# Kernel tuning notes

Hardware: AMD Instinct MI355X
Metric: run time of the kernel (lower is better)

## Reference

```python
import jax, jax.numpy as jnp
import numpy as np

WIN = 8      # window size
HEADS = 8    # num attention heads
LN_EPS = 1e-5


def setup_inputs() -> dict:
    key = jax.random.key(0)
    ks = jax.random.split(key, 4)
    B, C, H, W = 4, 256, 224, 224
    x = jax.random.normal(ks[0], (B, C, H, W), jnp.float32)
    # LayerNorm params (torch default init: weight=1, bias=0)
    ln_gamma = jnp.ones((C,), jnp.float32)
    ln_beta = jnp.zeros((C,), jnp.float32)
    # nn.MultiheadAttention: in_proj_weight xavier_uniform, biases zero
    s_in = float(np.sqrt(6.0 / (C + 3 * C)))
    w_qkv = jax.random.uniform(ks[1], (3 * C, C), jnp.float32, -s_in, s_in)
    b_qkv = jnp.zeros((3 * C,), jnp.float32)
    s_out = float(np.sqrt(6.0 / (C + C)))
    w_out = jax.random.uniform(ks[2], (C, C), jnp.float32, -s_out, s_out)
    b_out = jnp.zeros((C,), jnp.float32)
    return {"x": x, "ln_gamma": ln_gamma, "ln_beta": ln_beta,
            "w_qkv": w_qkv, "b_qkv": b_qkv, "w_out": w_out, "b_out": b_out}


def reference(x, ln_gamma, ln_beta, w_qkv, b_qkv, w_out, b_out):
    B, C, H, W = x.shape
    w = WIN
    h = HEADS
    d = C // h
    T = w * w  # tokens per window (64)
    # (B,C,H,W) -> (B,H,W,C); H,W divisible by win_size so F.pad is a no-op
    xb = jnp.transpose(x, (0, 2, 3, 1))
    # window_partition: (B*nW, T, C)
    win = xb.reshape(B, H // w, w, W // w, w, C)
    win = win.transpose(0, 1, 3, 2, 4, 5).reshape(-1, T, C)
    # LayerNorm over channel dim (same norm for q, k, v as in the source)
    mu = jnp.mean(win, axis=-1, keepdims=True)
    var = jnp.var(win, axis=-1, keepdims=True)  # biased, matches torch LN
    xn = (win - mu) * jax.lax.rsqrt(var + LN_EPS) * ln_gamma + ln_beta
    # fused QKV projection (torch MHA self-attn fast path)
    qkv = xn @ w_qkv.T + b_qkv          # (N, T, 3C)
    q, k, v = jnp.split(qkv, 3, axis=-1)

    def to_heads(t):  # (N, T, C) -> (N, h, T, d)
        return t.reshape(t.shape[0], T, h, d).transpose(0, 2, 1, 3)

    q, k, v = to_heads(q), to_heads(k), to_heads(v)
    scale = 1.0 / np.sqrt(d)
    scores = jnp.einsum('nhqd,nhkd->nhqk', q * scale, k)
    attn = jax.nn.softmax(scores, axis=-1)
    o = jnp.einsum('nhqk,nhkd->nhqd', attn, v)          # (N, h, T, d)
    o = o.transpose(0, 2, 1, 3).reshape(-1, T, C)       # merge heads
    o = o @ w_out.T + b_out
    # window_reverse: (B*nW, T, C) -> (B, H, W, C)
    out = o.reshape(B, H // w, W // w, w, w, C)
    out = out.transpose(0, 1, 3, 2, 4, 5).reshape(B, H, W, C)
    return jnp.transpose(out, (0, 3, 1, 2))  # (B, C, H, W)
```

## Files before the change

kernel.cpp:

```cpp
#include <hip/hip_runtime.h>
#include <hip/hip_fp16.h>

#define C_   256
#define H_   224
#define W_   224
#define HW_  (224 * 224)
#define NWH  28
#define NWW  28
#define NWIN 3136
#define NQUAD 784
#define NTILE 64
#define NFRAG (NTILE * 8 * 64)

#define XN_OFF (1ULL << 20)
#define O_OFF  (XN_OFF + (unsigned long long)NWIN * 32768ULL)
#define WS_NEED (O_OFF + (unsigned long long)NWIN * 32768ULL)

typedef _Float16 f16x8 __attribute__((ext_vector_type(8)));
typedef float    f32x4 __attribute__((ext_vector_type(4)));

__device__ __forceinline__ int xn_off(int row, int col) {
  return (row * 512 + col * 2) ^ ((((row & 7) ^ ((row >> 3) & 7))) << 4);
}
__device__ __forceinline__ int qk_off(int row, int col) {
  return (row * 64 + col * 2) ^ (((row >> 1) & 3) << 4);
}
__device__ __forceinline__ int vt_off(int d, int k) {
  return (d * 128 + k * 2) ^ ((d & 7) << 4);
}
__device__ __forceinline__ int p_off(int row, int col) {
  return (row * 128 + col * 2) ^ ((row & 7) << 4);
}
__device__ __forceinline__ _Float16* xn_at(char* s, int r, int c) { return (_Float16*)(s + xn_off(r, c)); }

__global__ void wcvt_kernel(const float* __restrict__ wqkv,
                            const float* __restrict__ wout,
                            _Float16* __restrict__ dst) {
  int f = blockIdx.x * blockDim.x + threadIdx.x;
  if (f >= NFRAG) return;
  int lane = f & 63, kk = (f >> 6) & 7, tile = f >> 9;
  int row = tile * 16 + (lane & 15);
  int col = kk * 32 + (lane >> 4) * 8;
  const float* src = (tile < 48) ? (wqkv + row * 256 + col)
                                 : (wout + (row - 768) * 256 + col);
  f32x4 a = *(const f32x4*)src;
  f32x4 b2 = *(const f32x4*)(src + 4);
  f16x8 r;
#pragma unroll
  for (int q = 0; q < 4; ++q) { r[q] = (_Float16)a[q]; r[q + 4] = (_Float16)b2[q]; }
  *(f16x8*)(dst + (size_t)f * 8) = r;
}

__global__ __launch_bounds__(512, 1) void prep_kernel(
    const float* __restrict__ x, const float* __restrict__ gamma,
    const float* __restrict__ beta, _Float16* __restrict__ xn_ws) {
  extern __shared__ char smem[];
  float* red = (float*)(smem + 131072);
  float* mrs = (float*)(smem + 147456);
  const int n0 = blockIdx.x;
  const int b  = n0 / 196;
  const int rem = n0 % 196;
  const int wh = rem / 7;
  const int wq = rem % 7;
  const int tid = threadIdx.x;
  const int px4 = (tid & 7) * 4;
  const int row = (tid >> 3) & 7;
  const int chg = tid >> 6;
  const int win = px4 >> 3;
  const int pc  = px4 & 7;
  char* xw = smem + win * 32768;

  {
    const size_t xoff = (size_t)b * C_ * HW_ + (size_t)(wh * 8 + row) * W_ + wq * 32 + px4;
    float s[4] = {0.f, 0.f, 0.f, 0.f}, q[4] = {0.f, 0.f, 0.f, 0.f};
#pragma unroll
    for (int cc = 0; cc < 32; ++cc) {
      const int ch = cc * 8 + chg;
      f32x4 v = *(const f32x4*)(x + xoff + (size_t)ch * HW_);
#pragma unroll
      for (int i = 0; i < 4; ++i) {
        *xn_at(xw, row * 8 + pc + i, ch) = (_Float16)v[i];
        s[i] += v[i]; q[i] += v[i] * v[i];
      }
    }
    const int tq = win * 64 + row * 8 + pc;
#pragma unroll
    for (int i = 0; i < 4; ++i) {
      red[(tq + i) * 8 + chg] = s[i];
      red[2048 + (tq + i) * 8 + chg] = q[i];
    }
  }
  __syncthreads();
  if (tid < 256) {
    float ss = 0.f, s2 = 0.f;
#pragma unroll
    for (int g = 0; g < 8; ++g) { ss += red[tid * 8 + g]; s2 += red[2048 + tid * 8 + g]; }
    float mu  = ss * (1.f / 256.f);
    float var = s2 * (1.f / 256.f) - mu * mu;
    mrs[tid]       = mu;
    mrs[256 + tid] = rsqrtf(var + 1e-5f);
  }
  __syncthreads();
  {
    char* dst = (char*)xn_ws + (size_t)((b * NWH + wh) * NWW + wq * 4) * 32768;
#pragma unroll
    for (int it = 0; it < 16; ++it) {
      const int a   = (it * 512 + tid) * 16;
      const int w2  = a >> 15;
      const int ab  = a & 32767;
      const int tok = ab >> 9;
      const int chb = ((ab & 511) ^ ((((tok & 7) ^ ((tok >> 3) & 7))) << 4)) >> 1;
      f16x8 hv = *(const f16x8*)(smem + a);
      const float mu = mrs[w2 * 64 + tok], rs = mrs[256 + w2 * 64 + tok];
      f32x4 g0 = *(const f32x4*)(gamma + chb), g1 = *(const f32x4*)(gamma + chb + 4);
      f32x4 b0 = *(const f32x4*)(beta + chb),  b1 = *(const f32x4*)(beta + chb + 4);
#pragma unroll
      for (int j = 0; j < 4; ++j) {
        hv[j]     = (_Float16)(((float)hv[j] - mu) * rs * g0[j] + b0[j]);
        hv[j + 4] = (_Float16)(((float)hv[j + 4] - mu) * rs * g1[j] + b1[j]);
      }
      *(f16x8*)(dst + a) = hv;
    }
  }
}

__global__ __launch_bounds__(512, 1) void megattn_kernel(
    const float* __restrict__ bqkv, const _Float16* __restrict__ w16,
    const _Float16* __restrict__ xn_ws, _Float16* __restrict__ o_ws) {
  extern __shared__ char smem[];
  const int tid = threadIdx.x;
  const int w = tid >> 6, lane = tid & 63, lr = lane & 15, lg = lane >> 4;
  const int winl = w >> 1;
  const int half = w & 1;
  const int r0   = half * 32;
  const int win  = blockIdx.x * 4 + winl;

  f16x8 af[2][8];
  {
    const char* xb = (const char*)xn_ws + (size_t)win * 32768;
#pragma unroll
    for (int mi = 0; mi < 2; ++mi)
#pragma unroll
      for (int kk = 0; kk < 8; ++kk)
        af[mi][kk] = *(const f16x8*)(xb + xn_off(r0 + mi * 16 + lr, kk * 32 + lg * 8));
  }

  char* scr   = smem + 49152 + winl * 12288;
  char* kbase = scr + 4096;
  char* vbase = scr + 8192;
  char* obuf  = smem + 98304 + winl * 4096;
  char* oblob = (char*)o_ws + (size_t)win * 32768;
  const float sc_q = 0.17677669529663687f;

#pragma unroll 1
  for (int h = 0; h < 8; ++h) {
    __syncthreads();
    {
      const char* s0 = (const char*)w16 + (size_t)(2 * h) * 8192;
      const char* s1 = (const char*)w16 + (size_t)(16 + 2 * h) * 8192;
      const char* s2 = (const char*)w16 + (size_t)(32 + 2 * h) * 8192;
#pragma unroll
      for (int it = 0; it < 2; ++it) {
        const int o = (it * 512 + tid) * 16;
        *(f32x4*)(smem + o)         = *(const f32x4*)(s0 + o);
        *(f32x4*)(smem + 16384 + o) = *(const f32x4*)(s1 + o);
        *(f32x4*)(smem + 32768 + o) = *(const f32x4*)(s2 + o);
      }
    }
    __syncthreads();

    f32x4 acc[6][2];
#pragma unroll
    for (int t = 0; t < 6; ++t)
#pragma unroll
      for (int mi = 0; mi < 2; ++mi) acc[t][mi] = (f32x4){0.f, 0.f, 0.f, 0.f};
#pragma unroll
    for (int kk = 0; kk < 8; ++kk) {
      const int fo = (kk * 64 + lane) * 16;
      f16x8 b0 = *(const f16x8*)(smem + fo);
      f16x8 b1 = *(const f16x8*)(smem + 8192 + fo);
      f16x8 b2 = *(const f16x8*)(smem + 16384 + fo);
      f16x8 b3 = *(const f16x8*)(smem + 24576 + fo);
      f16x8 b4 = *(const f16x8*)(smem + 32768 + fo);
      f16x8 b5 = *(const f16x8*)(smem + 40960 + fo);
#pragma unroll
      for (int mi = 0; mi < 2; ++mi) {
        acc[0][mi] = __builtin_amdgcn_mfma_f32_16x16x32_f16(af[mi][kk], b0, acc[0][mi], 0, 0, 0);
        acc[1][mi] = __builtin_amdgcn_mfma_f32_16x16x32_f16(af[mi][kk], b1, acc[1][mi], 0, 0, 0);
        acc[2][mi] = __builtin_amdgcn_mfma_f32_16x16x32_f16(af[mi][kk], b2, acc[2][mi], 0, 0, 0);
        acc[3][mi] = __builtin_amdgcn_mfma_f32_16x16x32_f16(af[mi][kk], b3, acc[3][mi], 0, 0, 0);
        acc[4][mi] = __builtin_amdgcn_mfma_f32_16x16x32_f16(af[mi][kk], b4, acc[4][mi], 0, 0, 0);
        acc[5][mi] = __builtin_amdgcn_mfma_f32_16x16x32_f16(af[mi][kk], b5, acc[5][mi], 0, 0, 0);
      }
    }
#pragma unroll
    for (int t2 = 0; t2 < 2; ++t2) {
      const float bq = bqkv[h * 32 + t2 * 16 + lr];
      const float bk = bqkv[256 + h * 32 + t2 * 16 + lr];
      const float bv = bqkv[512 + h * 32 + t2 * 16 + lr];
#pragma unroll
      for (int mi = 0; mi < 2; ++mi)
#pragma unroll
        for (int i = 0; i < 4; ++i) {
          const int trow = r0 + mi * 16 + lg * 4 + i;
          *(_Float16*)(scr + qk_off(trow, t2 * 16 + lr))   = (_Float16)((acc[t2][mi][i] + bq) * sc_q);
          *(_Float16*)(kbase + qk_off(trow, t2 * 16 + lr)) = (_Float16)(acc[2 + t2][mi][i] + bk);
          *(_Float16*)(vbase + vt_off(t2 * 16 + lr, trow)) = (_Float16)(acc[4 + t2][mi][i] + bv);
        }
    }
    __syncthreads();

    f16x8 qa[2], kb[4];
#pragma unroll
    for (int mi = 0; mi < 2; ++mi)
      qa[mi] = *(const f16x8*)(scr + qk_off(r0 + mi * 16 + lr, lg * 8));
#pragma unroll
    for (int ni = 0; ni < 4; ++ni)
      kb[ni] = *(const f16x8*)(kbase + qk_off(ni * 16 + lr, lg * 8));
    __syncthreads();

    float oinv[2][4];
#pragma unroll
    for (int mi = 0; mi < 2; ++mi) {
      f32x4 s4[4];
#pragma unroll
      for (int ni = 0; ni < 4; ++ni) {
        f32x4 z = {0.f, 0.f, 0.f, 0.f};
        s4[ni] = __builtin_amdgcn_mfma_f32_16x16x32_f16(qa[mi], kb[ni], z, 0, 0, 0);
      }
#pragma unroll
      for (int i = 0; i < 4; ++i) {
        float m = fmaxf(fmaxf(s4[0][i], s4[1][i]), fmaxf(s4[2][i], s4[3][i]));
        m = fmaxf(m, __shfl_xor(m, 1));
        m = fmaxf(m, __shfl_xor(m, 2));
        m = fmaxf(m, __shfl_xor(m, 4));
        m = fmaxf(m, __shfl_xor(m, 8));
        float s = 0.f;
#pragma unroll
        for (int ni = 0; ni < 4; ++ni) {
          float e = __expf(s4[ni][i] - m);
          s4[ni][i] = e;
          s += e;
        }
        s += __shfl_xor(s, 1);
        s += __shfl_xor(s, 2);
        s += __shfl_xor(s, 4);
        s += __shfl_xor(s, 8);
        oinv[mi][i] = 1.f / s;
      }
#pragma unroll
      for (int ni = 0; ni < 4; ++ni)
#pragma unroll
        for (int i = 0; i < 4; ++i)
          *(_Float16*)(scr + p_off(r0 + mi * 16 + lg * 4 + i, ni * 16 + lr)) = (_Float16)s4[ni][i];
    }
    f32x4 oacc[2][2];
#pragma unroll
    for (int mi = 0; mi < 2; ++mi)
#pragma unroll
      for (int nt2 = 0; nt2 < 2; ++nt2) oacc[mi][nt2] = (f32x4){0.f, 0.f, 0.f, 0.f};
#pragma unroll
    for (int ks2 = 0; ks2 < 2; ++ks2) {
      f16x8 pa[2];
#pragma unroll
      for (int mi = 0; mi < 2; ++mi)
        pa[mi] = *(const f16x8*)(scr + p_off(r0 + mi * 16 + lr, ks2 * 32 + lg * 8));
#pragma unroll
      for (int nt2 = 0; nt2 < 2; ++nt2) {
        f16x8 vb = *(const f16x8*)(vbase + vt_off(nt2 * 16 + lr, ks2 * 32 + lg * 8));
#pragma unroll
        for (int mi = 0; mi < 2; ++mi)
          oacc[mi][nt2] = __builtin_amdgcn_mfma_f32_16x16x32_f16(pa[mi], vb, oacc[mi][nt2], 0, 0, 0);
      }
    }
#pragma unroll
    for (int mi = 0; mi < 2; ++mi)
#pragma unroll
      for (int nt2 = 0; nt2 < 2; ++nt2)
#pragma unroll
        for (int i = 0; i < 4; ++i)
          *(_Float16*)(obuf + qk_off(r0 + mi * 16 + lg * 4 + i, nt2 * 16 + lr)) =
              (_Float16)(oacc[mi][nt2][i] * oinv[mi][i]);
#pragma unroll
    for (int j = 0; j < 2; ++j)
      *(f32x4*)(oblob + h * 4096 + half * 2048 + lane * 32 + j * 16) =
          *(const f32x4*)(obuf + half * 2048 + lane * 32 + j * 16);
  }
}

__device__ __forceinline__ f16x8 frag16(const _Float16* __restrict__ w16,
                                        int gt, int kk, int lane) {
  return *(const f16x8*)(w16 + ((size_t)((gt * 8 + kk) * 64 + lane)) * 8);
}
__global__ __launch_bounds__(512, 1) void outproj_kernel(
    const _Float16* __restrict__ o_ws, const _Float16* __restrict__ w16,
    const float* __restrict__ bout, float* __restrict__ out) {
  extern __shared__ char smem[];
  const int n0 = blockIdx.x;
  const int b  = n0 / 196;
  const int rem = n0 % 196;
  const int wh = rem / 7;
  const int wq = rem % 7;
  const int tid = threadIdx.x;
  const int w = tid >> 6, lane = tid & 63, lr = lane & 15, lg = lane >> 4;

  {
    const char* src = (const char*)o_ws + (size_t)((b * NWH + wh) * NWW + wq * 4) * 32768;
#pragma unroll
    for (int it = 0; it < 16; ++it) {
      const int off = (it * 512 + tid) * 16;
      *(f32x4*)(smem + off) = *(const f32x4*)(src + off);
    }
  }
  __syncthreads();

  f32x4 acc[4][2][4];
#pragma unroll
  for (int wi = 0; wi < 4; ++wi)
#pragma unroll
    for (int t = 0; t < 2; ++t)
#pragma unroll
      for (int mi = 0; mi < 4; ++mi) acc[wi][t][mi] = (f32x4){0.f, 0.f, 0.f, 0.f};

#pragma unroll
  for (int kk = 0; kk < 8; ++kk) {
    f16x8 bf0 = frag16(w16, 48 + w * 2 + 0, kk, lane);
    f16x8 bf1 = frag16(w16, 48 + w * 2 + 1, kk, lane);
#pragma unroll
    for (int wi = 0; wi < 4; ++wi) {
      f16x8 af[4];
#pragma unroll
      for (int mi = 0; mi < 4; ++mi)
        af[mi] = *(const f16x8*)(smem + wi * 32768 + kk * 4096 + qk_off(mi * 16 + lr, lg * 8));
#pragma unroll
      for (int mi = 0; mi < 4; ++mi) {
        acc[wi][0][mi] = __builtin_amdgcn_mfma_f32_16x16x32_f16(af[mi], bf0, acc[wi][0][mi], 0, 0, 0);
        acc[wi][1][mi] = __builtin_amdgcn_mfma_f32_16x16x32_f16(af[mi], bf1, acc[wi][1][mi], 0, 0, 0);
      }
    }
  }

#pragma unroll
  for (int ntl = 0; ntl < 2; ++ntl) {
    const int och = w * 32 + ntl * 16 + lr;
    const float bias = bout[och];
    float* ob = out + ((size_t)(b * C_ + och) * H_ + wh * 8) * W_ + wq * 32;
#pragma unroll
    for (int mi = 0; mi < 4; ++mi) {
      const int tb = mi * 16 + lg * 4;
      const int ro = (tb >> 3) * W_ + (tb & 7);
#pragma unroll
      for (int wi = 0; wi < 4; ++wi) {
        f32x4 ov;
#pragma unroll
        for (int i = 0; i < 4; ++i) ov[i] = acc[wi][ntl][mi][i] + bias;
        *(f32x4*)&ob[ro + wi * 8] = ov;
      }
    }
  }
}

extern "C" void kernel_launch(void* const* d_in, const int* in_sizes, int n_in,
                              void* d_out, int out_size, void* d_ws, size_t ws_size,
                              hipStream_t stream) {
  (void)in_sizes; (void)n_in; (void)out_size; (void)ws_size;
  const float* x     = (const float*)d_in[0];
  const float* gamma = (const float*)d_in[1];
  const float* beta  = (const float*)d_in[2];
  const float* wqkv  = (const float*)d_in[3];
  const float* bqkv  = (const float*)d_in[4];
  const float* wout  = (const float*)d_in[5];
  const float* bout  = (const float*)d_in[6];
  float* out = (float*)d_out;

  _Float16* w16   = (_Float16*)d_ws;
  _Float16* xn_ws = (_Float16*)((char*)d_ws + XN_OFF);
  _Float16* o_ws  = (_Float16*)((char*)d_ws + O_OFF);

  static int attr_set = 0;
  if (!attr_set) {
    (void)hipFuncSetAttribute((const void*)prep_kernel,
                              hipFuncAttributeMaxDynamicSharedMemorySize, 149504);
    (void)hipFuncSetAttribute((const void*)megattn_kernel,
                              hipFuncAttributeMaxDynamicSharedMemorySize, 114688);
    (void)hipFuncSetAttribute((const void*)outproj_kernel,
                              hipFuncAttributeMaxDynamicSharedMemorySize, 131072);
    attr_set = 1;
  }

  wcvt_kernel<<<NFRAG / 256, 256, 0, stream>>>(wqkv, wout, w16);
  prep_kernel<<<NQUAD, 512, 149504, stream>>>(x, gamma, beta, xn_ws);
  megattn_kernel<<<NQUAD, 512, 114688, stream>>>(bqkv, w16, xn_ws, o_ws);
  outproj_kernel<<<NQUAD, 512, 131072, stream>>>(o_ws, w16, bout, out);
}
```

Before: 411.8 us.

## Read QKV weight fragments from global memory and shrink attention blocks for occupancy

```diff
diff --git a/kernel.cpp b/kernel.cpp
--- a/kernel.cpp
+++ b/kernel.cpp
@@ -32,6 +32,11 @@
   return (row * 128 + col * 2) ^ ((row & 7) << 4);
 }
 __device__ __forceinline__ _Float16* xn_at(char* s, int r, int c) { return (_Float16*)(s + xn_off(r, c)); }
+
+__device__ __forceinline__ f16x8 frag16(const _Float16* __restrict__ w16,
+                                        int gt, int kk, int lane) {
+  return *(const f16x8*)(w16 + ((size_t)((gt * 8 + kk) * 64 + lane)) * 8);
+}
 
 __global__ void wcvt_kernel(const float* __restrict__ wqkv,
                             const float* __restrict__ wout,
@@ -124,7 +129,7 @@
   }
 }
 
-__global__ __launch_bounds__(512, 1) void megattn_kernel(
+__global__ __launch_bounds__(256, 4) void megattn_kernel(
     const float* __restrict__ bqkv, const _Float16* __restrict__ w16,
     const _Float16* __restrict__ xn_ws, _Float16* __restrict__ o_ws) {
   extern __shared__ char smem[];
@@ -133,7 +138,7 @@
   const int winl = w >> 1;
   const int half = w & 1;
   const int r0   = half * 32;
-  const int win  = blockIdx.x * 4 + winl;
+  const int win  = blockIdx.x * 2 + winl;
 
   f16x8 af[2][8];
   {
@@ -145,30 +150,15 @@
         af[mi][kk] = *(const f16x8*)(xb + xn_off(r0 + mi * 16 + lr, kk * 32 + lg * 8));
   }
 
-  char* scr   = smem + 49152 + winl * 12288;
+  char* scr   = smem + winl * 12288;
   char* kbase = scr + 4096;
   char* vbase = scr + 8192;
-  char* obuf  = smem + 98304 + winl * 4096;
+  char* obuf  = smem + 24576 + winl * 4096;
   char* oblob = (char*)o_ws + (size_t)win * 32768;
   const float sc_q = 0.17677669529663687f;
 
 #pragma unroll 1
   for (int h = 0; h < 8; ++h) {
-    __syncthreads();
-    {
-      const char* s0 = (const char*)w16 + (size_t)(2 * h) * 8192;
-      const char* s1 = (const char*)w16 + (size_t)(16 + 2 * h) * 8192;
-      const char* s2 = (const char*)w16 + (size_t)(32 + 2 * h) * 8192;
-#pragma unroll
-      for (int it = 0; it < 2; ++it) {
-        const int o = (it * 512 + tid) * 16;
-        *(f32x4*)(smem + o)         = *(const f32x4*)(s0 + o);
-        *(f32x4*)(smem + 16384 + o) = *(const f32x4*)(s1 + o);
-        *(f32x4*)(smem + 32768 + o) = *(const f32x4*)(s2 + o);
-      }
-    }
-    __syncthreads();
-
     f32x4 acc[6][2];
 #pragma unroll
     for (int t = 0; t < 6; ++t)
@@ -176,13 +166,12 @@
       for (int mi = 0; mi < 2; ++mi) acc[t][mi] = (f32x4){0.f, 0.f, 0.f, 0.f};
 #pragma unroll
     for (int kk = 0; kk < 8; ++kk) {
-      const int fo = (kk * 64 + lane) * 16;
-      f16x8 b0 = *(const f16x8*)(smem + fo);
-      f16x8 b1 = *(const f16x8*)(smem + 8192 + fo);
-      f16x8 b2 = *(const f16x8*)(smem + 16384 + fo);
-      f16x8 b3 = *(const f16x8*)(smem + 24576 + fo);
-      f16x8 b4 = *(const f16x8*)(smem + 32768 + fo);
-      f16x8 b5 = *(const f16x8*)(smem + 40960 + fo);
+      f16x8 b0 = frag16(w16, 2 * h,      kk, lane);
+      f16x8 b1 = frag16(w16, 2 * h + 1,  kk, lane);
+      f16x8 b2 = frag16(w16, 16 + 2 * h, kk, lane);
+      f16x8 b3 = frag16(w16, 17 + 2 * h, kk, lane);
+      f16x8 b4 = frag16(w16, 32 + 2 * h, kk, lane);
+      f16x8 b5 = frag16(w16, 33 + 2 * h, kk, lane);
 #pragma unroll
       for (int mi = 0; mi < 2; ++mi) {
         acc[0][mi] = __builtin_amdgcn_mfma_f32_16x16x32_f16(af[mi][kk], b0, acc[0][mi], 0, 0, 0);
@@ -193,6 +182,8 @@
         acc[5][mi] = __builtin_amdgcn_mfma_f32_16x16x32_f16(af[mi][kk], b5, acc[5][mi], 0, 0, 0);
       }
     }
+    __syncthreads();
+
 #pragma unroll
     for (int t2 = 0; t2 < 2; ++t2) {
       const float bq = bqkv[h * 32 + t2 * 16 + lr];
@@ -288,10 +279,6 @@
   }
 }
 
-__device__ __forceinline__ f16x8 frag16(const _Float16* __restrict__ w16,
-                                        int gt, int kk, int lane) {
-  return *(const f16x8*)(w16 + ((size_t)((gt * 8 + kk) * 64 + lane)) * 8);
-}
 __global__ __launch_bounds__(512, 1) void outproj_kernel(
     const _Float16* __restrict__ o_ws, const _Float16* __restrict__ w16,
     const float* __restrict__ bout, float* __restrict__ out) {
@@ -382,7 +369,7 @@
     (void)hipFuncSetAttribute((const void*)prep_kernel,
                               hipFuncAttributeMaxDynamicSharedMemorySize, 149504);
     (void)hipFuncSetAttribute((const void*)megattn_kernel,
-                              hipFuncAttributeMaxDynamicSharedMemorySize, 114688);
+                              hipFuncAttributeMaxDynamicSharedMemorySize, 32768);
     (void)hipFuncSetAttribute((const void*)outproj_kernel,
                               hipFuncAttributeMaxDynamicSharedMemorySize, 131072);
     attr_set = 1;
@@ -390,6 +377,6 @@
 
   wcvt_kernel<<<NFRAG / 256, 256, 0, stream>>>(wqkv, wout, w16);
   prep_kernel<<<NQUAD, 512, 149504, stream>>>(x, gamma, beta, xn_ws);
-  megattn_kernel<<<NQUAD, 512, 114688, stream>>>(bqkv, w16, xn_ws, o_ws);
+  megattn_kernel<<<NWIN / 2, 256, 32768, stream>>>(bqkv, w16, xn_ws, o_ws);
   outproj_kernel<<<NQUAD, 512, 131072, stream>>>(o_ws, w16, bout, out);
 }
```

After: 816.6 us. +98.3%, slower.

## Double-buffer per-head QKV weight tiles in LDS with register prefetch

Applied to the files above, without the earlier changes.

```diff
diff --git a/kernel.cpp b/kernel.cpp
--- a/kernel.cpp
+++ b/kernel.cpp
@@ -32,6 +32,17 @@
   return (row * 128 + col * 2) ^ ((row & 7) << 4);
 }
 __device__ __forceinline__ _Float16* xn_at(char* s, int r, int c) { return (_Float16*)(s + xn_off(r, c)); }
+
+__device__ __forceinline__ f16x8 frag16(const _Float16* __restrict__ w16,
+                                        int gt, int kk, int lane) {
+  return *(const f16x8*)(w16 + ((size_t)((gt * 8 + kk) * 64 + lane)) * 8);
+}
+
+__device__ __forceinline__ const char* wsrc(const char* w16b, int h, int c, int lane) {
+  const int reg = c >> 4;
+  const int off = (c & 15) << 10;
+  return w16b + (size_t)(reg * 16 + 2 * h) * 8192 + off + lane * 16;
+}
 
 __global__ void wcvt_kernel(const float* __restrict__ wqkv,
                             const float* __restrict__ wout,
@@ -134,6 +145,7 @@
   const int half = w & 1;
   const int r0   = half * 32;
   const int win  = blockIdx.x * 4 + winl;
+  const char* w16b = (const char*)w16;
 
   f16x8 af[2][8];
   {
@@ -145,30 +157,34 @@
         af[mi][kk] = *(const f16x8*)(xb + xn_off(r0 + mi * 16 + lr, kk * 32 + lg * 8));
   }
 
-  char* scr   = smem + 49152 + winl * 12288;
+  char* scr   = smem + 98304 + winl * 12288;
   char* kbase = scr + 4096;
   char* vbase = scr + 8192;
-  char* obuf  = smem + 98304 + winl * 4096;
+  char* obuf  = smem + 147456 + winl * 4096;
   char* oblob = (char*)o_ws + (size_t)win * 32768;
   const float sc_q = 0.17677669529663687f;
 
+  {
+    f32x4 r[6];
+#pragma unroll
+    for (int i = 0; i < 6; ++i)
+      r[i] = *(const f32x4*)wsrc(w16b, 0, w * 6 + i, lane);
+#pragma unroll
+    for (int i = 0; i < 6; ++i)
+      *(f32x4*)(smem + (w * 6 + i) * 1024 + lane * 16) = r[i];
+  }
+  __syncthreads();
+
 #pragma unroll 1
   for (int h = 0; h < 8; ++h) {
-    __syncthreads();
-    {
-      const char* s0 = (const char*)w16 + (size_t)(2 * h) * 8192;
-      const char* s1 = (const char*)w16 + (size_t)(16 + 2 * h) * 8192;
-      const char* s2 = (const char*)w16 + (size_t)(32 + 2 * h) * 8192;
-#pragma unroll
-      for (int it = 0; it < 2; ++it) {
-        const int o = (it * 512 + tid) * 16;
-        *(f32x4*)(smem + o)         = *(const f32x4*)(s0 + o);
-        *(f32x4*)(smem + 16384 + o) = *(const f32x4*)(s1 + o);
-        *(f32x4*)(smem + 32768 + o) = *(const f32x4*)(s2 + o);
-      }
-    }
-    __syncthreads();
-
+    f32x4 wreg[6];
+    if (h < 7) {
+#pragma unroll
+      for (int i = 0; i < 6; ++i)
+        wreg[i] = *(const f32x4*)wsrc(w16b, h + 1, w * 6 + i, lane);
+    }
+
+    char* bufb = smem + (h & 1) * 49152;
     f32x4 acc[6][2];
 #pragma unroll
     for (int t = 0; t < 6; ++t)
@@ -177,12 +193,12 @@
 #pragma unroll
     for (int kk = 0; kk < 8; ++kk) {
       const int fo = (kk * 64 + lane) * 16;
-      f16x8 b0 = *(const f16x8*)(smem + fo);
-      f16x8 b1 = *(const f16x8*)(smem + 8192 + fo);
-      f16x8 b2 = *(const f16x8*)(smem + 16384 + fo);
-      f16x8 b3 = *(const f16x8*)(smem + 24576 + fo);
-      f16x8 b4 = *(const f16x8*)(smem + 32768 + fo);
-      f16x8 b5 = *(const f16x8*)(smem + 40960 + fo);
+      f16x8 b0 = *(const f16x8*)(bufb + fo);
+      f16x8 b1 = *(const f16x8*)(bufb + 8192 + fo);
+      f16x8 b2 = *(const f16x8*)(bufb + 16384 + fo);
+      f16x8 b3 = *(const f16x8*)(bufb + 24576 + fo);
+      f16x8 b4 = *(const f16x8*)(bufb + 32768 + fo);
+      f16x8 b5 = *(const f16x8*)(bufb + 40960 + fo);
 #pragma unroll
       for (int mi = 0; mi < 2; ++mi) {
         acc[0][mi] = __builtin_amdgcn_mfma_f32_16x16x32_f16(af[mi][kk], b0, acc[0][mi], 0, 0, 0);
@@ -193,6 +209,15 @@
         acc[5][mi] = __builtin_amdgcn_mfma_f32_16x16x32_f16(af[mi][kk], b5, acc[5][mi], 0, 0, 0);
       }
     }
+    __syncthreads();
+
+    if (h < 7) {
+      char* nb = smem + ((h + 1) & 1) * 49152;
+#pragma unroll
+      for (int i = 0; i < 6; ++i)
+        *(f32x4*)(nb + (w * 6 + i) * 1024 + lane * 16) = wreg[i];
+    }
+
 #pragma unroll
     for (int t2 = 0; t2 < 2; ++t2) {
       const float bq = bqkv[h * 32 + t2 * 16 + lr];
@@ -288,10 +313,6 @@
   }
 }
 
-__device__ __forceinline__ f16x8 frag16(const _Float16* __restrict__ w16,
-                                        int gt, int kk, int lane) {
-  return *(const f16x8*)(w16 + ((size_t)((gt * 8 + kk) * 64 + lane)) * 8);
-}
 __global__ __launch_bounds__(512, 1) void outproj_kernel(
     const _Float16* __restrict__ o_ws, const _Float16* __restrict__ w16,
     const float* __restrict__ bout, float* __restrict__ out) {
@@ -382,7 +403,7 @@
     (void)hipFuncSetAttribute((const void*)prep_kernel,
                               hipFuncAttributeMaxDynamicSharedMemorySize, 149504);
     (void)hipFuncSetAttribute((const void*)megattn_kernel,
-                              hipFuncAttributeMaxDynamicSharedMemorySize, 114688);
+                              hipFuncAttributeMaxDynamicSharedMemorySize, 163840);
     (void)hipFuncSetAttribute((const void*)outproj_kernel,
                               hipFuncAttributeMaxDynamicSharedMemorySize, 131072);
     attr_set = 1;
@@ -390,6 +411,6 @@
 
   wcvt_kernel<<<NFRAG / 256, 256, 0, stream>>>(wqkv, wout, w16);
   prep_kernel<<<NQUAD, 512, 149504, stream>>>(x, gamma, beta, xn_ws);
-  megattn_kernel<<<NQUAD, 512, 114688, stream>>>(bqkv, w16, xn_ws, o_ws);
+  megattn_kernel<<<NQUAD, 512, 163840, stream>>>(bqkv, w16, xn_ws, o_ws);
   outproj_kernel<<<NQUAD, 512, 131072, stream>>>(o_ws, w16, bout, out);
 }
```

Result: slower. 533.7 us (+29.6%).
